# Kernel optimization log

Measured on AMD Instinct MI355X. Metric: run time of the kernel, lower is better.

Reference implementation:

```python
import jax, jax.numpy as jnp
import numpy as np

N_NODES = 100000
N_RAND_EDGES = 1200000
IN_DIM = 64
K = 10  # number of propagation hops


def setup_inputs() -> dict:
    key = jax.random.key(0)
    k1, k2, k3, k4 = jax.random.split(key, 4)
    feats = jax.random.normal(k1, (N_NODES, IN_DIM), dtype=jnp.float32)
    # xavier_uniform with sigmoid gain (=1.0) for s: bound = sqrt(6/(fan_in+fan_out))
    bound = float(np.sqrt(6.0 / (IN_DIM + 1)))
    s = jax.random.uniform(k2, (IN_DIM, 1), dtype=jnp.float32, minval=-bound, maxval=bound)
    src_r = jax.random.randint(k3, (N_RAND_EDGES,), 0, N_NODES)
    dst_r = jax.random.randint(k4, (N_RAND_EDGES,), 0, N_NODES)
    loops = jnp.arange(N_NODES)
    # append self-loops so every node has in_degree >= 1 (finite deg^-0.5)
    src = jnp.concatenate([src_r, loops]).astype(jnp.int64)
    dst = jnp.concatenate([dst_r, loops]).astype(jnp.int64)
    return {"feats": feats, "s": s, "src": src, "dst": dst}


def reference(feats, s, src, dst):
    n = feats.shape[0]
    ones = jnp.ones(src.shape[0], dtype=feats.dtype)
    degs = jax.ops.segment_sum(ones, dst, num_segments=n)  # in-degrees [N]
    norm = (degs ** -0.5)[:, None]  # [N,1]
    results = [feats]
    h = feats
    for _ in range(K):
        h = h * norm                                        # pre-scale
        h = jax.ops.segment_sum(h[src], dst, num_segments=n)  # copy_u + sum SpMM
        h = h * norm                                        # post-scale
        results.append(h)
    H = jnp.stack(results, axis=1)  # [N, K+1, D]
    S = jax.nn.sigmoid(jnp.einsum('nkd,do->nk', H, s))  # [N, K+1] gates
    return jnp.einsum('nk,nkd->nd', S, H)  # [N, D]
```

## Files before the change

kernel.cpp:

```cpp
#include <hip/hip_runtime.h>
#include <hip/hip_bf16.h>
#include <hip/hip_fp16.h>
#include <math.h>


#define DIM 64
#define BSH 9
#define BSZ 512
#define MAXNB 256
#define A2_CHUNK 4096

__global__ void zero_int_kernel(int* __restrict__ p, int n) {
    int i = blockIdx.x * blockDim.x + threadIdx.x;
    if (i < n) p[i] = 0;
}

__global__ void bin_count_kernel(const int* __restrict__ dst,
                                 int* __restrict__ binCount, int E) {
    __shared__ int lb[MAXNB];
    if (threadIdx.x < MAXNB) lb[threadIdx.x] = 0;
    __syncthreads();
    for (int e = blockIdx.x * blockDim.x + threadIdx.x; e < E;
         e += gridDim.x * blockDim.x) {
        atomicAdd(&lb[dst[e] >> BSH], 1);
    }
    __syncthreads();
    if (threadIdx.x < MAXNB && lb[threadIdx.x])
        atomicAdd(&binCount[threadIdx.x], lb[threadIdx.x]);
}

__global__ void binscan_kernel(const int* __restrict__ binCount,
                               int* __restrict__ binBase, int* __restrict__ tail,
                               int* __restrict__ rp, int NB, int N, int E) {
    __shared__ int lds[256];
    int t = threadIdx.x;
    int v = (t < NB) ? binCount[t] : 0;
    lds[t] = v;
    __syncthreads();
    for (int off = 1; off < 256; off <<= 1) {
        int x = (t >= off) ? lds[t - off] : 0;
        __syncthreads();
        lds[t] += x;
        __syncthreads();
    }
    int excl = lds[t] - v;
    if (t < NB) { binBase[t] = excl; tail[t] = excl; }
    if (t == 0) { binBase[NB] = E; rp[N] = E; }
}

__global__ void bin_scatter_kernel(const int* __restrict__ src,
                                   const int* __restrict__ dst,
                                   int* __restrict__ tail,
                                   int2* __restrict__ pairs, int E) {
    __shared__ int cnt[MAXNB];
    __shared__ int base[MAXNB];
    int t = threadIdx.x;
    int begE = blockIdx.x * A2_CHUNK;
    int endE = begE + A2_CHUNK; if (endE > E) endE = E;
    if (t < MAXNB) cnt[t] = 0;
    __syncthreads();
    for (int e = begE + t; e < endE; e += blockDim.x)
        atomicAdd(&cnt[dst[e] >> BSH], 1);
    __syncthreads();
    if (t < MAXNB) {
        int c = cnt[t];
        base[t] = c ? atomicAdd(&tail[t], c) : 0;
        cnt[t] = 0;
    }
    __syncthreads();
    for (int e = begE + t; e < endE; e += blockDim.x) {
        int d = dst[e];
        int b = d >> BSH;
        int pos = base[b] + atomicAdd(&cnt[b], 1);
        pairs[pos] = make_int2(src[e], d);
    }
}

__global__ void bucket_build_kernel(const int2* __restrict__ pairs,
                                    const int* __restrict__ binBase,
                                    int* __restrict__ col, int* __restrict__ rp,
                                    float* __restrict__ norm, int N) {
    __shared__ int degL[BSZ];
    __shared__ int off[BSZ];
    __shared__ int tmp[256];
    int b  = blockIdx.x;
    int lo = b << BSH;
    int cnt = N - lo; if (cnt > BSZ) cnt = BSZ;
    int t = threadIdx.x;
    degL[t] = 0; degL[t + 256] = 0;
    __syncthreads();
    int rbeg = binBase[b], rend = binBase[b + 1];
    for (int j = rbeg + t; j < rend; j += 256)
        atomicAdd(&degL[pairs[j].y - lo], 1);
    __syncthreads();
    int d0 = degL[2 * t], d1 = degL[2 * t + 1];
    int s2 = d0 + d1;
    tmp[t] = s2;
    __syncthreads();
    for (int o = 1; o < 256; o <<= 1) {
        int x = (t >= o) ? tmp[t - o] : 0;
        __syncthreads();
        tmp[t] += x;
        __syncthreads();
    }
    int e2 = tmp[t] - s2;
    off[2 * t]     = e2;
    off[2 * t + 1] = e2 + d0;
    __syncthreads();
    if (2 * t < cnt) {
        rp[lo + 2 * t] = rbeg + e2;
        norm[lo + 2 * t] = rsqrtf((float)d0);
    }
    if (2 * t + 1 < cnt) {
        rp[lo + 2 * t + 1] = rbeg + e2 + d0;
        norm[lo + 2 * t + 1] = rsqrtf((float)d1);
    }
    for (int j = rbeg + t; j < rend; j += 256) {
        int2 p = pairs[j];
        int slot = atomicAdd(&off[p.y - lo], 1);
        col[rbeg + slot] = p.x;
    }
}

__global__ void init_w0_kernel(const float* __restrict__ feats,
                               const float* __restrict__ norm,
                               __half* __restrict__ w, int N) {
    int n = blockIdx.x * (blockDim.x >> 6) + (threadIdx.x >> 6);
    int lane = threadIdx.x & 63;
    if (n >= N) return;
    size_t idx = ((size_t)n << 6) + lane;
    w[idx] = __float2half(feats[idx] * norm[n]);
}

__global__ void gather_hop_store_kernel(const __half* __restrict__ w,
                                        const int* __restrict__ rp,
                                        const int* __restrict__ col,
                                        const float* __restrict__ norm,
                                        __half* __restrict__ wnext, int N) {
    int n = blockIdx.x * (blockDim.x >> 6) + (threadIdx.x >> 6);
    if (n >= N) return;
    int lane  = threadIdx.x & 63;
    int e_sub = lane >> 3;
    int c     = lane & 7;

    int beg = rp[n];
    int end = rp[n + 1];
    int deg = end - beg;
    float nm = norm[n];

    int myc = 0;
    if (lane < deg) myc = col[beg + lane];

    float acc[8];
    #pragma unroll
    for (int i = 0; i < 8; ++i) acc[i] = 0.0f;

    int nfull = (deg < 64) ? deg : 64;

    {
        int cc0 = __shfl(myc, e_sub, 64);
        int cc1 = __shfl(myc, e_sub + 8, 64);
        float4 raw0 = *(const float4*)(w + ((size_t)cc0 << 6) + (c << 3));
        float4 raw1 = *(const float4*)(w + ((size_t)cc1 << 6) + (c << 3));
        if (e_sub < nfull) {
            const __half2* h2 = (const __half2*)&raw0;
            float2 f0 = __half22float2(h2[0]);
            float2 f1 = __half22float2(h2[1]);
            float2 f2 = __half22float2(h2[2]);
            float2 f3 = __half22float2(h2[3]);
            acc[0] += f0.x; acc[1] += f0.y;
            acc[2] += f1.x; acc[3] += f1.y;
            acc[4] += f2.x; acc[5] += f2.y;
            acc[6] += f3.x; acc[7] += f3.y;
        }
        if (e_sub + 8 < nfull) {
            const __half2* h2 = (const __half2*)&raw1;
            float2 f0 = __half22float2(h2[0]);
            float2 f1 = __half22float2(h2[1]);
            float2 f2 = __half22float2(h2[2]);
            float2 f3 = __half22float2(h2[3]);
            acc[0] += f0.x; acc[1] += f0.y;
            acc[2] += f1.x; acc[3] += f1.y;
            acc[4] += f2.x; acc[5] += f2.y;
            acc[6] += f3.x; acc[7] += f3.y;
        }
    }
    int ntrips = (nfull + 7) >> 3;
    for (int t = 2; t < ntrips; ++t) {
        int jj = e_sub + (t << 3);
        int cc = __shfl(myc, jj, 64);
        float4 raw = *(const float4*)(w + ((size_t)cc << 6) + (c << 3));
        if (jj < nfull) {
            const __half2* h2 = (const __half2*)&raw;
            float2 f0 = __half22float2(h2[0]);
            float2 f1 = __half22float2(h2[1]);
            float2 f2 = __half22float2(h2[2]);
            float2 f3 = __half22float2(h2[3]);
            acc[0] += f0.x; acc[1] += f0.y;
            acc[2] += f1.x; acc[3] += f1.y;
            acc[4] += f2.x; acc[5] += f2.y;
            acc[6] += f3.x; acc[7] += f3.y;
        }
    }
    for (int j = beg + 64 + e_sub; j < end; j += 8) {
        int cc = col[j];
        float4 raw = *(const float4*)(w + ((size_t)cc << 6) + (c << 3));
        const __half2* h2 = (const __half2*)&raw;
        float2 f0 = __half22float2(h2[0]);
        float2 f1 = __half22float2(h2[1]);
        float2 f2 = __half22float2(h2[2]);
        float2 f3 = __half22float2(h2[3]);
        acc[0] += f0.x; acc[1] += f0.y;
        acc[2] += f1.x; acc[3] += f1.y;
        acc[4] += f2.x; acc[5] += f2.y;
        acc[6] += f3.x; acc[7] += f3.y;
    }

    #pragma unroll
    for (int off = 8; off < 64; off <<= 1) {
        #pragma unroll
        for (int i = 0; i < 8; ++i) acc[i] += __shfl_xor(acc[i], off, 64);
    }

    if (e_sub == 0) {
        float n2 = nm * nm;
        __half2 hv[4];
        hv[0] = __floats2half2_rn(acc[0] * n2, acc[1] * n2);
        hv[1] = __floats2half2_rn(acc[2] * n2, acc[3] * n2);
        hv[2] = __floats2half2_rn(acc[4] * n2, acc[5] * n2);
        hv[3] = __floats2half2_rn(acc[6] * n2, acc[7] * n2);
        *(float4*)(wnext + ((size_t)n << 6) + (c << 3)) = *(const float4*)hv;
    }
}

__global__ void readout_kernel(const __half* __restrict__ wbase,
                               const float* __restrict__ norm,
                               const float* __restrict__ s,
                               float* __restrict__ out,
                               int N, int nk, size_t kstride) {
    int n = blockIdx.x * (blockDim.x >> 6) + (threadIdx.x >> 6);
    if (n >= N) return;
    int lane  = threadIdx.x & 63;
    int e_sub = lane >> 3;
    int c     = lane & 7;

    float4 sa = *(const float4*)(s + (c << 3));
    float4 sb = *(const float4*)(s + (c << 3) + 4);

    float inm = 1.0f / norm[n];
    size_t rowbase = ((size_t)n << 6) + (c << 3);

    float acc[8];
    #pragma unroll
    for (int i = 0; i < 8; ++i) acc[i] = 0.0f;

    #pragma unroll
    for (int iter = 0; iter < 2; ++iter) {
        int k = e_sub + iter * 8;
        float h[8];
        if (k < nk) {
            float4 raw = *(const float4*)(wbase + rowbase + (size_t)k * kstride);
            const __half2* h2 = (const __half2*)&raw;
            float2 f0 = __half22float2(h2[0]);
            float2 f1 = __half22float2(h2[1]);
            float2 f2 = __half22float2(h2[2]);
            float2 f3 = __half22float2(h2[3]);
            h[0] = f0.x * inm; h[1] = f0.y * inm;
            h[2] = f1.x * inm; h[3] = f1.y * inm;
            h[4] = f2.x * inm; h[5] = f2.y * inm;
            h[6] = f3.x * inm; h[7] = f3.y * inm;
        } else {
            #pragma unroll
            for (int i = 0; i < 8; ++i) h[i] = 0.0f;
        }
        float p = h[0] * sa.x + h[1] * sa.y + h[2] * sa.z + h[3] * sa.w
                + h[4] * sb.x + h[5] * sb.y + h[6] * sb.z + h[7] * sb.w;
        #pragma unroll
        for (int off = 1; off < 8; off <<= 1) p += __shfl_xor(p, off, 64);
        float gate = 1.0f / (1.0f + expf(-p));
        #pragma unroll
        for (int i = 0; i < 8; ++i) acc[i] += gate * h[i];
    }

    #pragma unroll
    for (int off = 8; off < 64; off <<= 1) {
        #pragma unroll
        for (int i = 0; i < 8; ++i) acc[i] += __shfl_xor(acc[i], off, 64);
    }

    if (e_sub == 0) {
        float4 o0 = make_float4(acc[0], acc[1], acc[2], acc[3]);
        float4 o1 = make_float4(acc[4], acc[5], acc[6], acc[7]);
        float4* o = (float4*)(out + rowbase);
        o[0] = o0; o[1] = o1;
    }
}

__global__ void init_kernel(const float* __restrict__ feats,
                            const float* __restrict__ norm,
                            const float* __restrict__ s,
                            float* __restrict__ out,
                            __half* __restrict__ w, int N) {
    int n = blockIdx.x * (blockDim.x >> 6) + (threadIdx.x >> 6);
    int lane = threadIdx.x & 63;
    if (n >= N) return;
    size_t idx = ((size_t)n << 6) + lane;
    float v = feats[idx];
    float p = v * s[lane];
    #pragma unroll
    for (int off = 32; off; off >>= 1) p += __shfl_xor(p, off, 64);
    float gate = 1.0f / (1.0f + expf(-p));
    out[idx] = gate * v;
    w[idx] = __float2half(v * norm[n]);
}

__global__ void gather_hop_kernel(const __half* __restrict__ w,
                                  const int* __restrict__ rp,
                                  const int* __restrict__ col,
                                  const float* __restrict__ norm,
                                  const float* __restrict__ s,
                                  float* __restrict__ out,
                                  __half* __restrict__ wnext,
                                  int N, int write_next) {
    int n = blockIdx.x * (blockDim.x >> 6) + (threadIdx.x >> 6);
    if (n >= N) return;
    int lane = threadIdx.x & 63;
    int e_sub = lane >> 3;
    int c     = lane & 7;

    int beg = rp[n];
    int end = rp[n + 1];

    float acc[8];
    #pragma unroll
    for (int i = 0; i < 8; ++i) acc[i] = 0.0f;

    for (int j = beg + e_sub; j < end; j += 8) {
        int cc = col[j];
        float4 raw = *(const float4*)(w + ((size_t)cc << 6) + (c << 3));
        const __half2* h2 = (const __half2*)&raw;
        float2 f0 = __half22float2(h2[0]);
        float2 f1 = __half22float2(h2[1]);
        float2 f2 = __half22float2(h2[2]);
        float2 f3 = __half22float2(h2[3]);
        acc[0] += f0.x; acc[1] += f0.y;
        acc[2] += f1.x; acc[3] += f1.y;
        acc[4] += f2.x; acc[5] += f2.y;
        acc[6] += f3.x; acc[7] += f3.y;
    }

    #pragma unroll
    for (int off = 8; off < 64; off <<= 1) {
        #pragma unroll
        for (int i = 0; i < 8; ++i) acc[i] += __shfl_xor(acc[i], off, 64);
    }

    float nm = norm[n];
    float v[8];
    #pragma unroll
    for (int i = 0; i < 8; ++i) v[i] = acc[i] * nm;

    float4 sa = *(const float4*)(s + (c << 3));
    float4 sb = *(const float4*)(s + (c << 3) + 4);
    float p = v[0] * sa.x + v[1] * sa.y + v[2] * sa.z + v[3] * sa.w
            + v[4] * sb.x + v[5] * sb.y + v[6] * sb.z + v[7] * sb.w;
    #pragma unroll
    for (int off = 1; off < 8; off <<= 1) p += __shfl_xor(p, off, 64);
    float gate = 1.0f / (1.0f + expf(-p));

    size_t base = ((size_t)n << 6) + (c << 3);
    if (e_sub == 0) {
        float4* o = (float4*)(out + base);
        float4 o0 = o[0], o1 = o[1];
        o0.x += gate * v[0]; o0.y += gate * v[1];
        o0.z += gate * v[2]; o0.w += gate * v[3];
        o1.x += gate * v[4]; o1.y += gate * v[5];
        o1.z += gate * v[6]; o1.w += gate * v[7];
        o[0] = o0; o[1] = o1;
    } else if (e_sub == 1 && write_next) {
        __half2 hv[4];
        hv[0] = __floats2half2_rn(v[0] * nm, v[1] * nm);
        hv[1] = __floats2half2_rn(v[2] * nm, v[3] * nm);
        hv[2] = __floats2half2_rn(v[4] * nm, v[5] * nm);
        hv[3] = __floats2half2_rn(v[6] * nm, v[7] * nm);
        *(float4*)(wnext + base) = *(const float4*)hv;
    }
}

extern "C" void kernel_launch(void* const* d_in, const int* in_sizes, int n_in,
                              void* d_out, int out_size, void* d_ws, size_t ws_size,
                              hipStream_t stream) {
    const float* feats = (const float*)d_in[0];
    const float* s     = (const float*)d_in[1];
    const int*   src   = (const int*)d_in[2];
    const int*   dst   = (const int*)d_in[3];
    float* out = (float*)d_out;

    const int N = in_sizes[0] / DIM;
    const int E = in_sizes[2];
    const int K = 10;
    const int NB = (N + BSZ - 1) >> BSH;

    const int BLK = 256;
    const int wavesPerBlk = BLK / 64;
    int nodeBlocks = (N + wavesPerBlk - 1) / wavesPerBlk;
    int a2Blocks = (E + A2_CHUNK - 1) / A2_CHUNK;

    size_t stateElems = (size_t)N * DIM;
    size_t intCount = (size_t)(N + 1) + E + 256 + 257 + 256;
    size_t need_full = (size_t)N * 4 + (size_t)(K + 1) * stateElems * 2
                     + intCount * 4 + (size_t)E * 8 + 64;
    int full = (ws_size >= need_full) ? 1 : 0;
    int nbuf = full ? (K + 1) : 2;

    float*  norm    = (float*)d_ws;
    __half* wbase   = (__half*)(norm + N);
    int*    rp      = (int*)(wbase + (size_t)nbuf * stateElems);
    int*    col     = rp + (N + 1);
    int*    binCount= col + E;
    int*    binBase = binCount + 256;
    int*    tail    = binBase + 257;
    size_t  poff    = (size_t)((char*)(tail + 256) - (char*)d_ws);
    poff = (poff + 7) & ~(size_t)7;
    int2*   pairs   = (int2*)((char*)d_ws + poff);

    zero_int_kernel<<<1, 256, 0, stream>>>(binCount, 256);
    bin_count_kernel<<<512, BLK, 0, stream>>>(dst, binCount, E);
    binscan_kernel<<<1, 256, 0, stream>>>(binCount, binBase, tail, rp, NB, N, E);
    bin_scatter_kernel<<<a2Blocks, BLK, 0, stream>>>(src, dst, tail, pairs, E);
    bucket_build_kernel<<<NB, 256, 0, stream>>>(pairs, binBase, col, rp, norm, N);

    if (full) {
        init_w0_kernel<<<nodeBlocks, BLK, 0, stream>>>(feats, norm, wbase, N);
        for (int k = 0; k < K; ++k) {
            const __half* cur = wbase + (size_t)k * stateElems;
            __half* nxt = wbase + (size_t)(k + 1) * stateElems;
            gather_hop_store_kernel<<<nodeBlocks, BLK, 0, stream>>>(cur, rp, col,
                                                                    norm, nxt, N);
        }
        readout_kernel<<<nodeBlocks, BLK, 0, stream>>>(wbase, norm, s, out,
                                                       N, K + 1, stateElems);
    } else {
        __half* wA = wbase;
        __half* wB = wbase + stateElems;
        init_kernel<<<nodeBlocks, BLK, 0, stream>>>(feats, norm, s, out, wA, N);
        __half* cur = wA;
        __half* nxt = wB;
        for (int k = 0; k < K; ++k) {
            int write_next = (k < K - 1) ? 1 : 0;
            gather_hop_kernel<<<nodeBlocks, BLK, 0, stream>>>(cur, rp, col, norm, s,
                                                              out, nxt, N, write_next);
            __half* t = cur; cur = nxt; nxt = t;
        }
    }
}
```

Baseline: 536.8 us.

## Map eight nodes per wavefront in gather and readout kernels

Both the hop gather kernel and the readout kernel now assign one node to each 8-lane group, so a wavefront handles 8 nodes instead of 1. This removes the cross-lane shuffle reductions over 64 lanes and the idle lanes for low-degree nodes (average in-degree is about 13). The cost is divergence inside a wave: the loop runs to the largest degree among its 8 nodes. Readout also loops over all hops per group and folds the inverse norm into the gate.

```diff
diff --git a/kernel.cpp b/kernel.cpp
--- a/kernel.cpp
+++ b/kernel.cpp
@@ -137,99 +137,74 @@
                                         const int* __restrict__ col,
                                         const float* __restrict__ norm,
                                         __half* __restrict__ wnext, int N) {
-    int n = blockIdx.x * (blockDim.x >> 6) + (threadIdx.x >> 6);
-    if (n >= N) return;
-    int lane  = threadIdx.x & 63;
-    int e_sub = lane >> 3;
-    int c     = lane & 7;
-
-    int beg = rp[n];
-    int end = rp[n + 1];
-    int deg = end - beg;
-    float nm = norm[n];
-
-    int myc = 0;
-    if (lane < deg) myc = col[beg + lane];
+    int wid  = (blockIdx.x * blockDim.x + threadIdx.x) >> 6;
+    int lane = threadIdx.x & 63;
+    int g    = lane >> 3;
+    int sub  = lane & 7;
+    int gbase = lane & 56;
+    int n    = (wid << 3) + g;
+    bool valid = (n < N);
+    int nc = valid ? n : (N - 1);
+
+    int beg = rp[nc];
+    int end = rp[nc + 1];
+    int deg = valid ? (end - beg) : 0;
+    float nm = norm[nc];
+
+    int maxdeg = deg;
+    maxdeg = max(maxdeg, __shfl_xor(maxdeg, 8, 64));
+    maxdeg = max(maxdeg, __shfl_xor(maxdeg, 16, 64));
+    maxdeg = max(maxdeg, __shfl_xor(maxdeg, 32, 64));
 
     float acc[8];
     #pragma unroll
     for (int i = 0; i < 8; ++i) acc[i] = 0.0f;
 
-    int nfull = (deg < 64) ? deg : 64;
-
-    {
-        int cc0 = __shfl(myc, e_sub, 64);
-        int cc1 = __shfl(myc, e_sub + 8, 64);
-        float4 raw0 = *(const float4*)(w + ((size_t)cc0 << 6) + (c << 3));
-        float4 raw1 = *(const float4*)(w + ((size_t)cc1 << 6) + (c << 3));
-        if (e_sub < nfull) {
-            const __half2* h2 = (const __half2*)&raw0;
-            float2 f0 = __half22float2(h2[0]);
-            float2 f1 = __half22float2(h2[1]);
-            float2 f2 = __half22float2(h2[2]);
-            float2 f3 = __half22float2(h2[3]);
-            acc[0] += f0.x; acc[1] += f0.y;
-            acc[2] += f1.x; acc[3] += f1.y;
-            acc[4] += f2.x; acc[5] += f2.y;
-            acc[6] += f3.x; acc[7] += f3.y;
+    const __half* wsub = w + (sub << 3);
+
+    for (int base = 0; base < maxdeg; base += 8) {
+        int i0 = beg + base + sub;
+        int c0 = (i0 < end) ? col[i0] : 0;
+        #pragma unroll
+        for (int jj = 0; jj < 8; jj += 2) {
+            if (base + jj >= maxdeg) break;
+            int ccA = __shfl(c0, gbase + jj, 64);
+            int ccB = __shfl(c0, gbase + jj + 1, 64);
+            float4 rA = *(const float4*)(wsub + ((size_t)ccA << 6));
+            float4 rB = *(const float4*)(wsub + ((size_t)ccB << 6));
+            if (base + jj < deg) {
+                const __half2* h2 = (const __half2*)&rA;
+                float2 f0 = __half22float2(h2[0]);
+                float2 f1 = __half22float2(h2[1]);
+                float2 f2 = __half22float2(h2[2]);
+                float2 f3 = __half22float2(h2[3]);
+                acc[0] += f0.x; acc[1] += f0.y;
+                acc[2] += f1.x; acc[3] += f1.y;
+                acc[4] += f2.x; acc[5] += f2.y;
+                acc[6] += f3.x; acc[7] += f3.y;
+            }
+            if (base + jj + 1 < deg) {
+                const __half2* h2 = (const __half2*)&rB;
+                float2 f0 = __half22float2(h2[0]);
+                float2 f1 = __half22float2(h2[1]);
+                float2 f2 = __half22float2(h2[2]);
+                float2 f3 = __half22float2(h2[3]);
+                acc[0] += f0.x; acc[1] += f0.y;
+                acc[2] += f1.x; acc[3] += f1.y;
+                acc[4] += f2.x; acc[5] += f2.y;
+                acc[6] += f3.x; acc[7] += f3.y;
+            }
         }
-        if (e_sub + 8 < nfull) {
-            const __half2* h2 = (const __half2*)&raw1;
-            float2 f0 = __half22float2(h2[0]);
-            float2 f1 = __half22float2(h2[1]);
-            float2 f2 = __half22float2(h2[2]);
-            float2 f3 = __half22float2(h2[3]);
-            acc[0] += f0.x; acc[1] += f0.y;
-            acc[2] += f1.x; acc[3] += f1.y;
-            acc[4] += f2.x; acc[5] += f2.y;
-            acc[6] += f3.x; acc[7] += f3.y;
-        }
-    }
-    int ntrips = (nfull + 7) >> 3;
-    for (int t = 2; t < ntrips; ++t) {
-        int jj = e_sub + (t << 3);
-        int cc = __shfl(myc, jj, 64);
-        float4 raw = *(const float4*)(w + ((size_t)cc << 6) + (c << 3));
-        if (jj < nfull) {
-            const __half2* h2 = (const __half2*)&raw;
-            float2 f0 = __half22float2(h2[0]);
-            float2 f1 = __half22float2(h2[1]);
-            float2 f2 = __half22float2(h2[2]);
-            float2 f3 = __half22float2(h2[3]);
-            acc[0] += f0.x; acc[1] += f0.y;
-            acc[2] += f1.x; acc[3] += f1.y;
-            acc[4] += f2.x; acc[5] += f2.y;
-            acc[6] += f3.x; acc[7] += f3.y;
-        }
-    }
-    for (int j = beg + 64 + e_sub; j < end; j += 8) {
-        int cc = col[j];
-        float4 raw = *(const float4*)(w + ((size_t)cc << 6) + (c << 3));
-        const __half2* h2 = (const __half2*)&raw;
-        float2 f0 = __half22float2(h2[0]);
-        float2 f1 = __half22float2(h2[1]);
-        float2 f2 = __half22float2(h2[2]);
-        float2 f3 = __half22float2(h2[3]);
-        acc[0] += f0.x; acc[1] += f0.y;
-        acc[2] += f1.x; acc[3] += f1.y;
-        acc[4] += f2.x; acc[5] += f2.y;
-        acc[6] += f3.x; acc[7] += f3.y;
-    }
-
-    #pragma unroll
-    for (int off = 8; off < 64; off <<= 1) {
-        #pragma unroll
-        for (int i = 0; i < 8; ++i) acc[i] += __shfl_xor(acc[i], off, 64);
-    }
-
-    if (e_sub == 0) {
+    }
+
+    if (valid) {
         float n2 = nm * nm;
         __half2 hv[4];
         hv[0] = __floats2half2_rn(acc[0] * n2, acc[1] * n2);
         hv[1] = __floats2half2_rn(acc[2] * n2, acc[3] * n2);
         hv[2] = __floats2half2_rn(acc[4] * n2, acc[5] * n2);
         hv[3] = __floats2half2_rn(acc[6] * n2, acc[7] * n2);
-        *(float4*)(wnext + ((size_t)n << 6) + (c << 3)) = *(const float4*)hv;
+        *(float4*)(wnext + ((size_t)n << 6) + (sub << 3)) = *(const float4*)hv;
     }
 }
 
@@ -238,60 +213,48 @@
                                const float* __restrict__ s,
                                float* __restrict__ out,
                                int N, int nk, size_t kstride) {
-    int n = blockIdx.x * (blockDim.x >> 6) + (threadIdx.x >> 6);
-    if (n >= N) return;
-    int lane  = threadIdx.x & 63;
-    int e_sub = lane >> 3;
-    int c     = lane & 7;
-
-    float4 sa = *(const float4*)(s + (c << 3));
-    float4 sb = *(const float4*)(s + (c << 3) + 4);
-
-    float inm = 1.0f / norm[n];
-    size_t rowbase = ((size_t)n << 6) + (c << 3);
+    int wid  = (blockIdx.x * blockDim.x + threadIdx.x) >> 6;
+    int lane = threadIdx.x & 63;
+    int g    = lane >> 3;
+    int sub  = lane & 7;
+    int n    = (wid << 3) + g;
+    bool valid = (n < N);
+    int nc = valid ? n : (N - 1);
+
+    float4 sa = *(const float4*)(s + (sub << 3));
+    float4 sb = *(const float4*)(s + (sub << 3) + 4);
+
+    float inm = 1.0f / norm[nc];
+    size_t rowoff = ((size_t)nc << 6) + (sub << 3);
 
     float acc[8];
     #pragma unroll
     for (int i = 0; i < 8; ++i) acc[i] = 0.0f;
 
-    #pragma unroll
-    for (int iter = 0; iter < 2; ++iter) {
-        int k = e_sub + iter * 8;
-        float h[8];
-        if (k < nk) {
-            float4 raw = *(const float4*)(wbase + rowbase + (size_t)k * kstride);
-            const __half2* h2 = (const __half2*)&raw;
-            float2 f0 = __half22float2(h2[0]);
-            float2 f1 = __half22float2(h2[1]);
-            float2 f2 = __half22float2(h2[2]);
-            float2 f3 = __half22float2(h2[3]);
-            h[0] = f0.x * inm; h[1] = f0.y * inm;
-            h[2] = f1.x * inm; h[3] = f1.y * inm;
-            h[4] = f2.x * inm; h[5] = f2.y * inm;
-            h[6] = f3.x * inm; h[7] = f3.y * inm;
-        } else {
-            #pragma unroll
-            for (int i = 0; i < 8; ++i) h[i] = 0.0f;
-        }
-        float p = h[0] * sa.x + h[1] * sa.y + h[2] * sa.z + h[3] * sa.w
-                + h[4] * sb.x + h[5] * sb.y + h[6] * sb.z + h[7] * sb.w;
-        #pragma unroll
-        for (int off = 1; off < 8; off <<= 1) p += __shfl_xor(p, off, 64);
-        float gate = 1.0f / (1.0f + expf(-p));
-        #pragma unroll
-        for (int i = 0; i < 8; ++i) acc[i] += gate * h[i];
-    }
-
-    #pragma unroll
-    for (int off = 8; off < 64; off <<= 1) {
-        #pragma unroll
-        for (int i = 0; i < 8; ++i) acc[i] += __shfl_xor(acc[i], off, 64);
-    }
-
-    if (e_sub == 0) {
+    for (int k = 0; k < nk; ++k) {
+        float4 raw = *(const float4*)(wbase + rowoff + (size_t)k * kstride);
+        const __half2* h2 = (const __half2*)&raw;
+        float2 f0 = __half22float2(h2[0]);
+        float2 f1 = __half22float2(h2[1]);
+        float2 f2 = __half22float2(h2[2]);
+        float2 f3 = __half22float2(h2[3]);
+        float p = f0.x * sa.x + f0.y * sa.y + f1.x * sa.z + f1.y * sa.w
+                + f2.x * sb.x + f2.y * sb.y + f3.x * sb.z + f3.y * sb.w;
+        p += __shfl_xor(p, 1, 64);
+        p += __shfl_xor(p, 2, 64);
+        p += __shfl_xor(p, 4, 64);
+        float gate = 1.0f / (1.0f + expf(-p * inm));
+        float g2 = gate * inm;
+        acc[0] += g2 * f0.x; acc[1] += g2 * f0.y;
+        acc[2] += g2 * f1.x; acc[3] += g2 * f1.y;
+        acc[4] += g2 * f2.x; acc[5] += g2 * f2.y;
+        acc[6] += g2 * f3.x; acc[7] += g2 * f3.y;
+    }
+
+    if (valid) {
         float4 o0 = make_float4(acc[0], acc[1], acc[2], acc[3]);
         float4 o1 = make_float4(acc[4], acc[5], acc[6], acc[7]);
-        float4* o = (float4*)(out + rowbase);
+        float4* o = (float4*)(out + rowoff);
         o[0] = o0; o[1] = o1;
     }
 }
@@ -403,7 +366,8 @@
 
     const int BLK = 256;
     const int wavesPerBlk = BLK / 64;
-    int nodeBlocks = (N + wavesPerBlk - 1) / wavesPerBlk;
+    int nodeBlocks  = (N + wavesPerBlk - 1) / wavesPerBlk;
+    int nodeBlocks8 = (N + wavesPerBlk * 8 - 1) / (wavesPerBlk * 8);
     int a2Blocks = (E + A2_CHUNK - 1) / A2_CHUNK;
 
     size_t stateElems = (size_t)N * DIM;
@@ -435,11 +399,11 @@
         for (int k = 0; k < K; ++k) {
             const __half* cur = wbase + (size_t)k * stateElems;
             __half* nxt = wbase + (size_t)(k + 1) * stateElems;
-            gather_hop_store_kernel<<<nodeBlocks, BLK, 0, stream>>>(cur, rp, col,
-                                                                    norm, nxt, N);
+            gather_hop_store_kernel<<<nodeBlocks8, BLK, 0, stream>>>(cur, rp, col,
+                                                                     norm, nxt, N);
         }
-        readout_kernel<<<nodeBlocks, BLK, 0, stream>>>(wbase, norm, s, out,
-                                                       N, K + 1, stateElems);
+        readout_kernel<<<nodeBlocks8, BLK, 0, stream>>>(wbase, norm, s, out,
+                                                        N, K + 1, stateElems);
     } else {
         __half* wA = wbase;
         __half* wB = wbase + stateElems;
```

Result: faster. 442.3 us (-17.6%).
